# Performance work log

Measured on AMD Instinct MI355X. Metric: run time of the kernel, lower is better.

## Reference

```python
import jax, jax.numpy as jnp
import numpy as np

N, D, E, K = 8192, 1024, 16, 2
CAP = 1024  # capacity_per_expert


def setup_inputs() -> dict:
    key = jax.random.key(0)
    k1, k2, k3 = jax.random.split(key, 3)
    return {
        "moe_inp": jax.random.normal(k1, (N, D), dtype=jnp.float32),
        "gate_w": jax.random.normal(k2, (D, E), dtype=jnp.float32) * 0.02,
        "gate_b": jnp.zeros((E,), dtype=jnp.float32),
        "expert_w": jax.random.normal(k3, (E, D, D), dtype=jnp.float32) * 0.02,
        "expert_b": jnp.zeros((E, D), dtype=jnp.float32),
    }


def _capacity_keep_mask(expert_id, slot_score, num_experts, capacity):
    """For each flattened (token, k) slot assigned to an expert, keep only the
    `capacity` slots with the highest token score (gate_score.max over k),
    matching the argsort-based drop in _fmoe_limited_global_forward."""
    nslots = expert_id.shape[0]
    # sort slots by (expert asc, score desc)
    order = jnp.lexsort((-slot_score, expert_id))
    counts = jnp.bincount(expert_id, length=num_experts)
    starts = jnp.concatenate([jnp.zeros((1,), counts.dtype), jnp.cumsum(counts)[:-1]])
    pos_in_expert = jnp.arange(nslots) - starts[expert_id[order]]
    keep_sorted = pos_in_expert < capacity
    return jnp.zeros((nslots,), dtype=bool).at[order].set(keep_sorted)


def reference(moe_inp, gate_w, gate_b, expert_w, expert_b):
    n, d = moe_inp.shape
    e = expert_w.shape[0]
    # NaiveGate: linear -> top-k -> softmax over the k selected logits
    logits = moe_inp @ gate_w + gate_b                       # [N, E]
    top_v, top_i = jax.lax.top_k(logits, K)                  # [N, K]
    gate_score = jax.nn.softmax(top_v, axis=-1)              # [N, K]

    expert_id = top_i.reshape(-1)                            # [N*K]
    token_id = jnp.arange(n * K) // K                        # [N*K]
    mask_scores = gate_score.max(axis=-1)                    # [N] per-token score
    slot_score = mask_scores[token_id]                       # [N*K]

    keep = _capacity_keep_mask(expert_id, slot_score, e, CAP).reshape(n, K)

    # expert forward: FMoELinear y = x @ W_e^T + b_e (dense over experts, then gather)
    all_out = jnp.einsum('nd,efd->nef', moe_inp, expert_w) + expert_b  # [N, E, D]
    y = jnp.take_along_axis(all_out, top_i[:, :, None], axis=1)        # [N, K, D]
    # dropped (over-capacity) slots pass the scattered input through unchanged
    y = jnp.where(keep[:, :, None], y, moe_inp[:, None, :])
    # combine: bmm(gate_score [N,1,K], y [N,K,D]) -> [N, D]
    return jnp.einsum('nk,nkd->nd', gate_score, y)
```

## Files before the change

kernel.cpp:

```cpp
#include <hip/hip_runtime.h>
#include <hip/hip_bf16.h>
#include <math.h>

#define N_TOK 8192
#define DIM   1024
#define NEXP  16
#define TOPK  2
#define CAPE  1024
#define NSLOT (N_TOK*TOPK)

typedef __attribute__((ext_vector_type(8))) short     short8;
typedef __attribute__((ext_vector_type(4))) float     floatx4;
typedef __attribute__((ext_vector_type(4))) unsigned short ushort4v;

__device__ __forceinline__ unsigned short f2bf(float f) {
    unsigned u = __float_as_uint(f);
    u += 0x7FFFu + ((u >> 16) & 1u);
    return (unsigned short)(u >> 16);
}

#define GLOAD_LDS16(g, l) __builtin_amdgcn_global_load_lds( \
    (const __attribute__((address_space(1))) unsigned int*)(g), \
    (__attribute__((address_space(3))) unsigned int*)(l), 16, 0, 0)

__global__ void gwt_kernel(const float* __restrict__ gw, float* __restrict__ gwT) {
    int i = blockIdx.x * 256 + threadIdx.x;
    if (i >= DIM * NEXP) return;
    int d = i >> 4, e = i & 15;
    gwT[e * DIM + d] = gw[i];
}

__global__ __launch_bounds__(256) void gate_kernel(
        const float* __restrict__ x,
        const float* __restrict__ gwT,
        const float* __restrict__ gb,
        int* __restrict__ slot_expert,
        unsigned long long* __restrict__ slot_key,
        float* __restrict__ slot_gate,
        unsigned short* __restrict__ Xb) {
    const int t    = blockIdx.x * 4 + (threadIdx.x >> 6);
    const int lane = threadIdx.x & 63;

    const floatx4* xr = (const floatx4*)(x + (size_t)t * DIM);
    ushort4v* Xb4 = (ushort4v*)Xb + (size_t)t * 256;
    floatx4 xv[4];
#pragma unroll
    for (int i = 0; i < 4; i++) {
        xv[i] = xr[lane + i * 64];
        ushort4v o;
        o[0] = f2bf(xv[i][0]); o[1] = f2bf(xv[i][1]);
        o[2] = f2bf(xv[i][2]); o[3] = f2bf(xv[i][3]);
        Xb4[lane + i * 64] = o;
    }

    float acc[NEXP];
#pragma unroll
    for (int e = 0; e < NEXP; e++) {
        const floatx4* wr = (const floatx4*)(gwT + (size_t)e * DIM);
        float a = 0.f;
#pragma unroll
        for (int i = 0; i < 4; i++) {
            floatx4 w = wr[lane + i * 64];
            a += xv[i][0]*w[0] + xv[i][1]*w[1] + xv[i][2]*w[2] + xv[i][3]*w[3];
        }
        acc[e] = a;
    }
#pragma unroll
    for (int off = 32; off > 0; off >>= 1) {
#pragma unroll
        for (int e = 0; e < NEXP; e++) acc[e] += __shfl_down(acc[e], off, 64);
    }
    if (lane == 0) {
        float v0 = -1e30f; int i0 = 0;
#pragma unroll
        for (int e = 0; e < NEXP; e++) {
            float v = acc[e] + gb[e];
            acc[e] = v;
            if (v > v0) { v0 = v; i0 = e; }
        }
        float v1 = -1e30f; int i1 = 0;
#pragma unroll
        for (int e = 0; e < NEXP; e++) {
            if (e != i0 && acc[e] > v1) { v1 = acc[e]; i1 = e; }
        }
        float e1 = expf(v1 - v0);
        float den = 1.f + e1;
        float g0 = 1.f / den;
        float g1 = e1 / den;
        unsigned sb = __float_as_uint(g0);
        int s0 = 2 * t, s1 = 2 * t + 1;
        slot_expert[s0] = i0; slot_expert[s1] = i1;
        slot_gate[s0]   = g0; slot_gate[s1]   = g1;
        unsigned long long hi = ((unsigned long long)sb) << 32;
        slot_key[s0] = hi | (unsigned)(0xFFFFFFFFu - (unsigned)s0);
        slot_key[s1] = hi | (unsigned)(0xFFFFFFFFu - (unsigned)s1);
    }
}

__global__ __launch_bounds__(256) void bucket_kernel(
        const int* __restrict__ slot_expert,
        const unsigned long long* __restrict__ slot_key,
        int* __restrict__ counts,
        unsigned long long* __restrict__ buckets) {
    __shared__ int lcnt[NEXP];
    __shared__ int lbase[NEXP];
    const int tid = threadIdx.x;
    const int s = blockIdx.x * 256 + tid;
    if (tid < NEXP) lcnt[tid] = 0;
    __syncthreads();
    const int e = slot_expert[s];
    const unsigned long long key = slot_key[s];
    const int lpos = atomicAdd(&lcnt[e], 1);
    __syncthreads();
    if (tid < NEXP) lbase[tid] = lcnt[tid] ? atomicAdd(&counts[tid], lcnt[tid]) : 0;
    __syncthreads();
    buckets[(size_t)e * NSLOT + lbase[e] + lpos] = key;
}

__global__ __launch_bounds__(256) void keep_wave_kernel(
        const int* __restrict__ slot_expert,
        const unsigned long long* __restrict__ slot_key,
        const int* __restrict__ counts,
        const unsigned long long* __restrict__ buckets,
        int* __restrict__ slot_keep) {
    const int wv   = threadIdx.x >> 6;
    const int lane = threadIdx.x & 63;
    const int s    = blockIdx.x * 4 + wv;
    const int e    = slot_expert[s];
    const int c    = counts[e];
    int kp = 1;
    if (c > CAPE) {
        const unsigned long long k = slot_key[s];
        const unsigned long long* bk = buckets + (size_t)e * NSLOT;
        int rank = 0;
        for (int i = lane; i < c; i += 64) rank += (bk[i] > k) ? 1 : 0;
#pragma unroll
        for (int off = 32; off > 0; off >>= 1) rank += __shfl_down(rank, off, 64);
        kp = (__shfl(rank, 0, 64) < CAPE) ? 1 : 0;
    }
    if (lane == 0) slot_keep[s] = kp;
}

__global__ __launch_bounds__(256) void compact_kernel(
        const int* __restrict__ slot_expert,
        const int* __restrict__ slot_keep,
        int* __restrict__ ecount,
        int* __restrict__ elist,
        int* __restrict__ slot_pos) {
    __shared__ int lcnt[NEXP];
    __shared__ int lbase[NEXP];
    const int tid = threadIdx.x;
    const int s = blockIdx.x * 256 + tid;
    if (tid < NEXP) lcnt[tid] = 0;
    __syncthreads();
    const int e  = slot_expert[s];
    const int kp = slot_keep[s];
    int lpos = 0;
    if (kp) lpos = atomicAdd(&lcnt[e], 1);
    __syncthreads();
    if (tid < NEXP) lbase[tid] = lcnt[tid] ? atomicAdd(&ecount[tid], lcnt[tid]) : 0;
    __syncthreads();
    if (kp) {
        int p = lbase[e] + lpos;
        elist[e * CAPE + p] = s;
        if (slot_pos) slot_pos[s] = e * CAPE + p;
    }
}

__global__ void base_kernel(const float* __restrict__ x,
                            const int* __restrict__ keep,
                            const float* __restrict__ gate,
                            float* __restrict__ out) {
    int i = blockIdx.x * blockDim.x + threadIdx.x;
    int t = i >> 8;
    float c = 0.f;
    if (!keep[2 * t])     c += gate[2 * t];
    if (!keep[2 * t + 1]) c += gate[2 * t + 1];
    floatx4 v = ((const floatx4*)x)[i];
    ((floatx4*)out)[i] = v * c;
}

__global__ void cvt_kernel(const float* __restrict__ src,
                           unsigned short* __restrict__ dst, int n4) {
    int i = blockIdx.x * blockDim.x + threadIdx.x;
    if (i >= n4) return;
    floatx4 v = ((const floatx4*)src)[i];
    ushort4v o;
    o[0] = f2bf(v[0]); o[1] = f2bf(v[1]); o[2] = f2bf(v[2]); o[3] = f2bf(v[3]);
    ((ushort4v*)dst)[i] = o;
}

template <bool STORE_YS>
__global__ __launch_bounds__(256)
void moe_gemm(const unsigned short* __restrict__ Xb,
              const unsigned short* __restrict__ Wb,
              const float* __restrict__ eb,
              const int* __restrict__ elist,
              const int* __restrict__ ecount,
              const float* __restrict__ slot_gate,
              float* __restrict__ ys,
              float* __restrict__ out) {
    __shared__ unsigned short As[128 * 32];
    __shared__ unsigned short Bs[128 * 32];

    const int e  = blockIdx.z;
    const int ne = ecount[e];
    const int m0 = blockIdx.y * 128;
    if (m0 >= ne) return;
    const int n0   = blockIdx.x * 128;
    const int wv   = threadIdx.x >> 6;
    const int lane = threadIdx.x & 63;
    const int q    = lane >> 4;
    const int l15  = lane & 15;

    const int jblk = (lane & 3) ^ ((lane >> 3) & 3);
    const unsigned short* gA[2];
    const unsigned short* gB[2];
    int chunk[2];
#pragma unroll
    for (int c = 0; c < 2; c++) {
        int ch = wv * 2 + c;
        chunk[c] = ch;
        int arow = ch * 16 + (lane >> 2);
        int m    = m0 + arow;
        int slot = elist[e * CAPE + (m < ne ? m : 0)];
        int tok  = slot >> 1;
        gA[c] = Xb + (size_t)tok * DIM + jblk * 8;
        int frow = n0 + arow;
        gB[c] = Wb + (size_t)e * DIM * DIM + (size_t)frow * DIM + jblk * 8;
    }

    const int wm = (wv & 1) * 64;
    const int wn = (wv >> 1) * 64;
    const int kswz = ((l15 >> 1) & 3);
    floatx4 acc[4][4] = {};

    for (int k0 = 0; k0 < DIM; k0 += 32) {
        __syncthreads();
#pragma unroll
        for (int c = 0; c < 2; c++) {
            GLOAD_LDS16(gA[c] + k0, &As[chunk[c] * 512]);
            GLOAD_LDS16(gB[c] + k0, &Bs[chunk[c] * 512]);
        }
        __syncthreads();

        short8 af[4], bf[4];
        const int koff = (q ^ kswz) * 8;
#pragma unroll
        for (int fi = 0; fi < 4; fi++)
            af[fi] = *(const short8*)&As[(wm + fi * 16 + l15) * 32 + koff];
#pragma unroll
        for (int fj = 0; fj < 4; fj++)
            bf[fj] = *(const short8*)&Bs[(wn + fj * 16 + l15) * 32 + koff];
#pragma unroll
        for (int fi = 0; fi < 4; fi++)
#pragma unroll
            for (int fj = 0; fj < 4; fj++)
                acc[fi][fj] = __builtin_amdgcn_mfma_f32_16x16x32_bf16(
                    af[fi], bf[fj], acc[fi][fj], 0, 0, 0);
    }

    float ebv[4];
#pragma unroll
    for (int fj = 0; fj < 4; fj++)
        ebv[fj] = eb[e * DIM + n0 + wn + fj * 16 + l15];
#pragma unroll
    for (int fi = 0; fi < 4; fi++) {
        const int mrow = m0 + wm + fi * 16 + q * 4;
#pragma unroll
        for (int r = 0; r < 4; r++) {
            int m = mrow + r;
            if (m >= ne) continue;
            if (STORE_YS) {
                float* yrow = ys + ((size_t)e * CAPE + m) * DIM + n0 + wn;
#pragma unroll
                for (int fj = 0; fj < 4; fj++)
                    yrow[fj * 16 + l15] = acc[fi][fj][r] + ebv[fj];
            } else {
                int slot = elist[e * CAPE + m];
                int tok  = slot >> 1;
                float g  = slot_gate[slot];
                float* orow = out + (size_t)tok * DIM + n0 + wn;
#pragma unroll
                for (int fj = 0; fj < 4; fj++)
                    atomicAdd(orow + fj * 16 + l15, g * (acc[fi][fj][r] + ebv[fj]));
            }
        }
    }
}

__global__ void combine_kernel(const float* __restrict__ x,
                               const float* __restrict__ ys,
                               const int* __restrict__ keep,
                               const int* __restrict__ pos,
                               const float* __restrict__ gate,
                               float* __restrict__ out) {
    int i = blockIdx.x * 256 + threadIdx.x;
    int t = i >> 8;
    int c = i & 255;
    int s0 = 2 * t, s1 = s0 + 1;
    floatx4 xv = ((const floatx4*)x)[i];
    float g0 = gate[s0], g1 = gate[s1];
    floatx4 r;
    if (keep[s0]) {
        floatx4 y0 = ((const floatx4*)ys)[((size_t)pos[s0] << 8) + c];
        r = y0 * g0;
    } else r = xv * g0;
    if (keep[s1]) {
        floatx4 y1 = ((const floatx4*)ys)[((size_t)pos[s1] << 8) + c];
        r += y1 * g1;
    } else r += xv * g1;
    ((floatx4*)out)[i] = r;
}

extern "C" void kernel_launch(void* const* d_in, const int* in_sizes, int n_in,
                              void* d_out, int out_size, void* d_ws, size_t ws_size,
                              hipStream_t stream) {
    const float* x  = (const float*)d_in[0];
    const float* gw = (const float*)d_in[1];
    const float* gb = (const float*)d_in[2];
    const float* ew = (const float*)d_in[3];
    const float* eb = (const float*)d_in[4];
    float* out = (float*)d_out;

    char* ws = (char*)d_ws;
    int* counts      = (int*)(ws + 0);
    int* ecount      = (int*)(ws + 64);
    int* slot_expert = (int*)(ws + 256);
    int* slot_keep   = (int*)(ws + 65792);
    float* slot_gate = (float*)(ws + 131328);
    unsigned long long* slot_key = (unsigned long long*)(ws + 196864);
    unsigned long long* buckets  = (unsigned long long*)(ws + 327936);
    int* elist       = (int*)(ws + 2425088);
    float* gwT       = (float*)(ws + 2490624);
    unsigned short* Xb = (unsigned short*)(ws + 2556160);
    unsigned short* Wb = (unsigned short*)(ws + 19333376);
    int* slot_pos    = (int*)(ws + 52887808);
    int* ecount2     = (int*)(ws + 52953088);
    float* ys        = (float*)(ws + 52953344);
    const size_t WS_NEED_YS = 52953344ull + (size_t)NEXP * CAPE * DIM * 4;

    const bool ys_path = (ws_size >= WS_NEED_YS);
    (void)ecount2;

    hipMemsetAsync(ws, 0, 256, stream);

    gwt_kernel <<<64, 256, 0, stream>>>(gw, gwT);
    gate_kernel<<<N_TOK / 4, 256, 0, stream>>>(x, gwT, gb, slot_expert, slot_key,
                                               slot_gate, Xb);
    bucket_kernel<<<NSLOT / 256, 256, 0, stream>>>(slot_expert, slot_key, counts, buckets);
    keep_wave_kernel<<<NSLOT / 4, 256, 0, stream>>>(slot_expert, slot_key, counts,
                                                    buckets, slot_keep);
    compact_kernel<<<NSLOT / 256, 256, 0, stream>>>(slot_expert, slot_keep, ecount, elist,
                                                    ys_path ? slot_pos : nullptr);
    cvt_kernel<<<(NEXP * DIM * DIM / 4) / 256, 256, 0, stream>>>(ew, Wb, NEXP * DIM * DIM / 4);

    if (ys_path) {
        moe_gemm<true><<<dim3(8, 8, 16), 256, 0, stream>>>(Xb, Wb, eb, elist, ecount,
                                                           slot_gate, ys, out);
        combine_kernel<<<N_TOK, 256, 0, stream>>>(x, ys, slot_keep, slot_pos,
                                                  slot_gate, out);
    } else {
        base_kernel<<<(N_TOK * DIM / 4) / 256, 256, 0, stream>>>(x, slot_keep,
                                                                 slot_gate, out);
        moe_gemm<false><<<dim3(8, 8, 16), 256, 0, stream>>>(Xb, Wb, eb, elist, ecount,
                                                            slot_gate, nullptr, out);
    }
}
```

Baseline: 266.1 us.

## Rewrite expert GEMM with 256x256 tiles, double-buffered LDS, and interleaved MFMA scheduling

The expert GEMM moves from 128x128 tiles with K=32 and a single LDS buffer to 256x256 tiles with K=64, 512 threads and two LDS buffers. Global-to-LDS loads for the next k-step are issued between MFMA phases, using raw s_barrier, explicit vmcnt waits and s_setprio, so loads overlap compute. The larger tiles cut global reloads of X and W per FLOP but use 128 KB of LDS, more accumulator registers, and give a grid of only 256 blocks, which risks low occupancy and wave underutilisation. A new XOR swizzle is applied on the 64-wide rows to avoid LDS bank conflicts.

```diff
diff --git a/kernel.cpp b/kernel.cpp
--- a/kernel.cpp
+++ b/kernel.cpp
@@ -22,6 +22,8 @@
 #define GLOAD_LDS16(g, l) __builtin_amdgcn_global_load_lds( \
     (const __attribute__((address_space(1))) unsigned int*)(g), \
     (__attribute__((address_space(3))) unsigned int*)(l), 16, 0, 0)
+
+#define RAW_BARRIER() asm volatile("s_barrier" ::: "memory")
 
 __global__ void gwt_kernel(const float* __restrict__ gw, float* __restrict__ gwT) {
     int i = blockIdx.x * 256 + threadIdx.x;
@@ -191,7 +193,7 @@
 }
 
 template <bool STORE_YS>
-__global__ __launch_bounds__(256)
+__global__ __launch_bounds__(512, 2)
 void moe_gemm(const unsigned short* __restrict__ Xb,
               const unsigned short* __restrict__ Wb,
               const float* __restrict__ eb,
@@ -200,79 +202,157 @@
               const float* __restrict__ slot_gate,
               float* __restrict__ ys,
               float* __restrict__ out) {
-    __shared__ unsigned short As[128 * 32];
-    __shared__ unsigned short Bs[128 * 32];
+    __shared__ unsigned short As[2][256 * 64];
+    __shared__ unsigned short Bs[2][256 * 64];
 
     const int e  = blockIdx.z;
     const int ne = ecount[e];
-    const int m0 = blockIdx.y * 128;
+    const int m0 = blockIdx.y * 256;
     if (m0 >= ne) return;
-    const int n0   = blockIdx.x * 128;
-    const int wv   = threadIdx.x >> 6;
-    const int lane = threadIdx.x & 63;
+    const int n0   = blockIdx.x * 256;
+    const int tid  = threadIdx.x;
+    const int wv   = tid >> 6;
+    const int lane = tid & 63;
     const int q    = lane >> 4;
     const int l15  = lane & 15;
-
-    const int jblk = (lane & 3) ^ ((lane >> 3) & 3);
-    const unsigned short* gA[2];
-    const unsigned short* gB[2];
-    int chunk[2];
-#pragma unroll
-    for (int c = 0; c < 2; c++) {
-        int ch = wv * 2 + c;
-        chunk[c] = ch;
-        int arow = ch * 16 + (lane >> 2);
+    const int wr   = wv & 1;
+    const int wc   = wv >> 1;
+
+    const int srow = wv * 8 + (lane >> 3);
+    const int jsrc = (lane & 7) ^ (srow & 7);
+    const unsigned short* gA[4];
+    const unsigned short* gB[4];
+#pragma unroll
+    for (int g = 0; g < 4; g++) {
+        int arow = g * 64 + srow;
         int m    = m0 + arow;
         int slot = elist[e * CAPE + (m < ne ? m : 0)];
-        int tok  = slot >> 1;
-        gA[c] = Xb + (size_t)tok * DIM + jblk * 8;
-        int frow = n0 + arow;
-        gB[c] = Wb + (size_t)e * DIM * DIM + (size_t)frow * DIM + jblk * 8;
-    }
-
-    const int wm = (wv & 1) * 64;
-    const int wn = (wv >> 1) * 64;
-    const int kswz = ((l15 >> 1) & 3);
-    floatx4 acc[4][4] = {};
-
-    for (int k0 = 0; k0 < DIM; k0 += 32) {
-        __syncthreads();
-#pragma unroll
-        for (int c = 0; c < 2; c++) {
-            GLOAD_LDS16(gA[c] + k0, &As[chunk[c] * 512]);
-            GLOAD_LDS16(gB[c] + k0, &Bs[chunk[c] * 512]);
-        }
-        __syncthreads();
-
-        short8 af[4], bf[4];
-        const int koff = (q ^ kswz) * 8;
+        gA[g] = Xb + (size_t)(slot >> 1) * DIM + jsrc * 8;
+        gB[g] = Wb + (size_t)e * DIM * DIM + (size_t)(n0 + arow) * DIM + jsrc * 8;
+    }
+
+#define STAGE_A4(b, k0) do { \
+    GLOAD_LDS16(gA[0] + (k0), &As[b][0 * 4096 + wv * 512]); \
+    GLOAD_LDS16(gA[1] + (k0), &As[b][1 * 4096 + wv * 512]); \
+    GLOAD_LDS16(gA[2] + (k0), &As[b][2 * 4096 + wv * 512]); \
+    GLOAD_LDS16(gA[3] + (k0), &As[b][3 * 4096 + wv * 512]); } while (0)
+#define STAGE_B2(b, g0, k0) do { \
+    GLOAD_LDS16(gB[g0] + (k0),     &Bs[b][(g0) * 4096 + wv * 512]); \
+    GLOAD_LDS16(gB[(g0)+1] + (k0), &Bs[b][((g0)+1) * 4096 + wv * 512]); } while (0)
+
+    STAGE_A4(0, 0);
+    STAGE_B2(0, 0, 0); STAGE_B2(0, 2, 0);
+    STAGE_A4(1, 64);
+    asm volatile("s_waitcnt vmcnt(4)" ::: "memory");
+    __builtin_amdgcn_sched_barrier(0);
+    RAW_BARRIER();
+
+    const int swz0 = (q ^ (l15 & 7)) * 8;
+    const int swz1 = ((4 + q) ^ (l15 & 7)) * 8;
+    const int arow_s = (wr * 128 + l15) * 64;
+    const int brow_s = (wc * 64 + l15) * 64;
+
+    floatx4 acc[8][4] = {};
+    short8 a[4][2], b[4][2];
+
+    for (int t = 0; t < 16; t++) {
+        const unsigned short* A_ = &As[t & 1][0];
+        const unsigned short* B_ = &Bs[t & 1][0];
+        const int nb = (t & 1) ^ 1;
+        const int k1 = (t + 1) * 64;
+        const int k2 = (t + 2) * 64;
+
+#pragma unroll
+        for (int fi = 0; fi < 4; fi++) {
+            a[fi][0] = *(const short8*)(A_ + arow_s + fi * 1024 + swz0);
+            a[fi][1] = *(const short8*)(A_ + arow_s + fi * 1024 + swz1);
+        }
+#pragma unroll
+        for (int fj = 0; fj < 2; fj++) {
+            b[fj][0] = *(const short8*)(B_ + brow_s + fj * 1024 + swz0);
+            b[fj][1] = *(const short8*)(B_ + brow_s + fj * 1024 + swz1);
+        }
+        if (t + 1 < 16) STAGE_B2(nb, 0, k1);
+        RAW_BARRIER();
+        __builtin_amdgcn_s_setprio(1);
 #pragma unroll
         for (int fi = 0; fi < 4; fi++)
-            af[fi] = *(const short8*)&As[(wm + fi * 16 + l15) * 32 + koff];
-#pragma unroll
-        for (int fj = 0; fj < 4; fj++)
-            bf[fj] = *(const short8*)&Bs[(wn + fj * 16 + l15) * 32 + koff];
+#pragma unroll
+            for (int fj = 0; fj < 2; fj++) {
+                acc[fi][fj] = __builtin_amdgcn_mfma_f32_16x16x32_bf16(
+                    a[fi][0], b[fj][0], acc[fi][fj], 0, 0, 0);
+                acc[fi][fj] = __builtin_amdgcn_mfma_f32_16x16x32_bf16(
+                    a[fi][1], b[fj][1], acc[fi][fj], 0, 0, 0);
+            }
+        __builtin_amdgcn_s_setprio(0);
+        RAW_BARRIER();
+
+#pragma unroll
+        for (int fj = 2; fj < 4; fj++) {
+            b[fj][0] = *(const short8*)(B_ + brow_s + fj * 1024 + swz0);
+            b[fj][1] = *(const short8*)(B_ + brow_s + fj * 1024 + swz1);
+        }
+        if (t + 1 < 16) STAGE_B2(nb, 2, k1);
+        RAW_BARRIER();
+        __builtin_amdgcn_s_setprio(1);
 #pragma unroll
         for (int fi = 0; fi < 4; fi++)
 #pragma unroll
-            for (int fj = 0; fj < 4; fj++)
+            for (int fj = 2; fj < 4; fj++) {
                 acc[fi][fj] = __builtin_amdgcn_mfma_f32_16x16x32_bf16(
-                    af[fi], bf[fj], acc[fi][fj], 0, 0, 0);
-    }
+                    a[fi][0], b[fj][0], acc[fi][fj], 0, 0, 0);
+                acc[fi][fj] = __builtin_amdgcn_mfma_f32_16x16x32_bf16(
+                    a[fi][1], b[fj][1], acc[fi][fj], 0, 0, 0);
+            }
+        __builtin_amdgcn_s_setprio(0);
+        RAW_BARRIER();
+
+#pragma unroll
+        for (int fi = 0; fi < 4; fi++) {
+            a[fi][0] = *(const short8*)(A_ + arow_s + 4096 + fi * 1024 + swz0);
+            a[fi][1] = *(const short8*)(A_ + arow_s + 4096 + fi * 1024 + swz1);
+        }
+        RAW_BARRIER();
+        __builtin_amdgcn_s_setprio(1);
+#pragma unroll
+        for (int fi = 0; fi < 4; fi++)
+#pragma unroll
+            for (int fj = 0; fj < 4; fj++) {
+                acc[fi + 4][fj] = __builtin_amdgcn_mfma_f32_16x16x32_bf16(
+                    a[fi][0], b[fj][0], acc[fi + 4][fj], 0, 0, 0);
+                acc[fi + 4][fj] = __builtin_amdgcn_mfma_f32_16x16x32_bf16(
+                    a[fi][1], b[fj][1], acc[fi + 4][fj], 0, 0, 0);
+            }
+        __builtin_amdgcn_s_setprio(0);
+        RAW_BARRIER();
+
+        if (t + 1 < 16) {
+            if (t + 2 < 16) {
+                STAGE_A4(t & 1, k2);
+                asm volatile("s_waitcnt vmcnt(4)" ::: "memory");
+            } else {
+                asm volatile("s_waitcnt vmcnt(0)" ::: "memory");
+            }
+            __builtin_amdgcn_sched_barrier(0);
+            RAW_BARRIER();
+        }
+    }
+#undef STAGE_A4
+#undef STAGE_B2
 
     float ebv[4];
 #pragma unroll
     for (int fj = 0; fj < 4; fj++)
-        ebv[fj] = eb[e * DIM + n0 + wn + fj * 16 + l15];
-#pragma unroll
-    for (int fi = 0; fi < 4; fi++) {
-        const int mrow = m0 + wm + fi * 16 + q * 4;
+        ebv[fj] = eb[e * DIM + n0 + wc * 64 + fj * 16 + l15];
+#pragma unroll
+    for (int fi = 0; fi < 8; fi++) {
+        const int mrow = m0 + wr * 128 + fi * 16 + q * 4;
 #pragma unroll
         for (int r = 0; r < 4; r++) {
             int m = mrow + r;
             if (m >= ne) continue;
             if (STORE_YS) {
-                float* yrow = ys + ((size_t)e * CAPE + m) * DIM + n0 + wn;
+                float* yrow = ys + ((size_t)e * CAPE + m) * DIM + n0 + wc * 64;
 #pragma unroll
                 for (int fj = 0; fj < 4; fj++)
                     yrow[fj * 16 + l15] = acc[fi][fj][r] + ebv[fj];
@@ -280,7 +360,7 @@
                 int slot = elist[e * CAPE + m];
                 int tok  = slot >> 1;
                 float g  = slot_gate[slot];
-                float* orow = out + (size_t)tok * DIM + n0 + wn;
+                float* orow = out + (size_t)tok * DIM + n0 + wc * 64;
 #pragma unroll
                 for (int fj = 0; fj < 4; fj++)
                     atomicAdd(orow + fj * 16 + l15, g * (acc[fi][fj][r] + ebv[fj]));
@@ -356,14 +436,14 @@
     cvt_kernel<<<(NEXP * DIM * DIM / 4) / 256, 256, 0, stream>>>(ew, Wb, NEXP * DIM * DIM / 4);
 
     if (ys_path) {
-        moe_gemm<true><<<dim3(8, 8, 16), 256, 0, stream>>>(Xb, Wb, eb, elist, ecount,
+        moe_gemm<true><<<dim3(4, 4, 16), 512, 0, stream>>>(Xb, Wb, eb, elist, ecount,
                                                            slot_gate, ys, out);
         combine_kernel<<<N_TOK, 256, 0, stream>>>(x, ys, slot_keep, slot_pos,
                                                   slot_gate, out);
     } else {
         base_kernel<<<(N_TOK * DIM / 4) / 256, 256, 0, stream>>>(x, slot_keep,
                                                                  slot_gate, out);
-        moe_gemm<false><<<dim3(8, 8, 16), 256, 0, stream>>>(Xb, Wb, eb, elist, ecount,
+        moe_gemm<false><<<dim3(4, 4, 16), 512, 0, stream>>>(Xb, Wb, eb, elist, ecount,
                                                             slot_gate, nullptr, out);
     }
 }
```

Result: faster. 244.5 us (-8.1%).

## Double-buffer MoE GEMM LDS tiles with 256x128 blocks of 8 waves

Applied to the files above, without the earlier changes.

Rewrites the expert GEMM main loop to double-buffer A/B tiles in LDS, keeping two stages of global-to-LDS loads in flight using explicit vmcnt waits and raw barriers. The block tile grows to 256 rows by 128 columns with 512 threads (8 waves), which halves the grid's M dimension and doubles reuse of each weight tile. MFMA sections are given higher wave priority. LDS use doubles, and the hand-written waitcnt/barrier ordering is fragile if the compiler reorders loads.

```diff
diff --git a/kernel.cpp b/kernel.cpp
--- a/kernel.cpp
+++ b/kernel.cpp
@@ -22,6 +22,8 @@
 #define GLOAD_LDS16(g, l) __builtin_amdgcn_global_load_lds( \
     (const __attribute__((address_space(1))) unsigned int*)(g), \
     (__attribute__((address_space(3))) unsigned int*)(l), 16, 0, 0)
+
+#define RAW_BARRIER() asm volatile("s_barrier" ::: "memory")
 
 __global__ void gwt_kernel(const float* __restrict__ gw, float* __restrict__ gwT) {
     int i = blockIdx.x * 256 + threadIdx.x;
@@ -191,7 +193,7 @@
 }
 
 template <bool STORE_YS>
-__global__ __launch_bounds__(256)
+__global__ __launch_bounds__(512, 4)
 void moe_gemm(const unsigned short* __restrict__ Xb,
               const unsigned short* __restrict__ Wb,
               const float* __restrict__ eb,
@@ -200,65 +202,79 @@
               const float* __restrict__ slot_gate,
               float* __restrict__ ys,
               float* __restrict__ out) {
-    __shared__ unsigned short As[128 * 32];
-    __shared__ unsigned short Bs[128 * 32];
+    __shared__ unsigned short As[2][256 * 32];
+    __shared__ unsigned short Bs[2][128 * 32];
 
     const int e  = blockIdx.z;
     const int ne = ecount[e];
-    const int m0 = blockIdx.y * 128;
+    const int m0 = blockIdx.y * 256;
     if (m0 >= ne) return;
     const int n0   = blockIdx.x * 128;
-    const int wv   = threadIdx.x >> 6;
-    const int lane = threadIdx.x & 63;
+    const int tid  = threadIdx.x;
+    const int wv   = tid >> 6;
+    const int lane = tid & 63;
     const int q    = lane >> 4;
     const int l15  = lane & 15;
-
-    const int jblk = (lane & 3) ^ ((lane >> 3) & 3);
-    const unsigned short* gA[2];
-    const unsigned short* gB[2];
-    int chunk[2];
-#pragma unroll
-    for (int c = 0; c < 2; c++) {
-        int ch = wv * 2 + c;
-        chunk[c] = ch;
-        int arow = ch * 16 + (lane >> 2);
-        int m    = m0 + arow;
+    const int wm   = (wv >> 1) * 64;
+    const int wn   = (wv & 1) * 64;
+
+    const int srow = wv * 16 + (lane >> 2);
+    const int jsrc = (lane & 3) ^ ((lane >> 3) & 3);
+    const unsigned short* gA0;
+    const unsigned short* gA1;
+    {
+        int m = m0 + srow;
         int slot = elist[e * CAPE + (m < ne ? m : 0)];
-        int tok  = slot >> 1;
-        gA[c] = Xb + (size_t)tok * DIM + jblk * 8;
-        int frow = n0 + arow;
-        gB[c] = Wb + (size_t)e * DIM * DIM + (size_t)frow * DIM + jblk * 8;
-    }
-
-    const int wm = (wv & 1) * 64;
-    const int wn = (wv >> 1) * 64;
-    const int kswz = ((l15 >> 1) & 3);
+        gA0 = Xb + (size_t)(slot >> 1) * DIM + jsrc * 8;
+        m = m0 + 128 + srow;
+        slot = elist[e * CAPE + (m < ne ? m : 0)];
+        gA1 = Xb + (size_t)(slot >> 1) * DIM + jsrc * 8;
+    }
+    const unsigned short* gB0 =
+        Wb + (size_t)e * DIM * DIM + (size_t)(n0 + srow) * DIM + jsrc * 8;
+
+#define STAGE(b, k0) do { \
+    GLOAD_LDS16(gA0 + (k0), &As[b][(wv * 16) * 32]); \
+    GLOAD_LDS16(gA1 + (k0), &As[b][(128 + wv * 16) * 32]); \
+    GLOAD_LDS16(gB0 + (k0), &Bs[b][(wv * 16) * 32]); } while (0)
+
+    STAGE(0, 0);
+    STAGE(1, 32);
+
+    const int swz  = (q ^ ((l15 >> 1) & 3)) * 8;
+    const int aoff = (wm + l15) * 32 + swz;
+    const int boff = (wn + l15) * 32 + swz;
+
     floatx4 acc[4][4] = {};
-
-    for (int k0 = 0; k0 < DIM; k0 += 32) {
-        __syncthreads();
-#pragma unroll
-        for (int c = 0; c < 2; c++) {
-            GLOAD_LDS16(gA[c] + k0, &As[chunk[c] * 512]);
-            GLOAD_LDS16(gB[c] + k0, &Bs[chunk[c] * 512]);
-        }
-        __syncthreads();
-
-        short8 af[4], bf[4];
-        const int koff = (q ^ kswz) * 8;
-#pragma unroll
-        for (int fi = 0; fi < 4; fi++)
-            af[fi] = *(const short8*)&As[(wm + fi * 16 + l15) * 32 + koff];
-#pragma unroll
-        for (int fj = 0; fj < 4; fj++)
-            bf[fj] = *(const short8*)&Bs[(wn + fj * 16 + l15) * 32 + koff];
+    short8 a[4], b[4];
+
+    for (int t = 0; t < 32; t++) {
+        const int cur = t & 1;
+        if (t == 31) { asm volatile("s_waitcnt vmcnt(0)" ::: "memory"); }
+        else         { asm volatile("s_waitcnt vmcnt(3)" ::: "memory"); }
+        __builtin_amdgcn_sched_barrier(0);
+        RAW_BARRIER();
+
+        const unsigned short* A_ = &As[cur][0];
+        const unsigned short* B_ = &Bs[cur][0];
+#pragma unroll
+        for (int fi = 0; fi < 4; fi++) a[fi] = *(const short8*)(A_ + aoff + fi * 512);
+#pragma unroll
+        for (int fj = 0; fj < 4; fj++) b[fj] = *(const short8*)(B_ + boff + fj * 512);
+
+        __builtin_amdgcn_s_setprio(1);
 #pragma unroll
         for (int fi = 0; fi < 4; fi++)
 #pragma unroll
             for (int fj = 0; fj < 4; fj++)
                 acc[fi][fj] = __builtin_amdgcn_mfma_f32_16x16x32_bf16(
-                    af[fi], bf[fj], acc[fi][fj], 0, 0, 0);
-    }
+                    a[fi], b[fj], acc[fi][fj], 0, 0, 0);
+        __builtin_amdgcn_s_setprio(0);
+        RAW_BARRIER();
+
+        if (t + 2 < 32) STAGE(cur, (t + 2) * 32);
+    }
+#undef STAGE
 
     float ebv[4];
 #pragma unroll
@@ -356,14 +372,14 @@
     cvt_kernel<<<(NEXP * DIM * DIM / 4) / 256, 256, 0, stream>>>(ew, Wb, NEXP * DIM * DIM / 4);
 
     if (ys_path) {
-        moe_gemm<true><<<dim3(8, 8, 16), 256, 0, stream>>>(Xb, Wb, eb, elist, ecount,
+        moe_gemm<true><<<dim3(8, 4, 16), 512, 0, stream>>>(Xb, Wb, eb, elist, ecount,
                                                            slot_gate, ys, out);
         combine_kernel<<<N_TOK, 256, 0, stream>>>(x, ys, slot_keep, slot_pos,
                                                   slot_gate, out);
     } else {
         base_kernel<<<(N_TOK * DIM / 4) / 256, 256, 0, stream>>>(x, slot_keep,
                                                                  slot_gate, out);
-        moe_gemm<false><<<dim3(8, 8, 16), 256, 0, stream>>>(Xb, Wb, eb, elist, ecount,
+        moe_gemm<false><<<dim3(8, 4, 16), 512, 0, stream>>>(Xb, Wb, eb, elist, ecount,
                                                             slot_gate, nullptr, out);
     }
 }
```

New measurement: 243.8 us. -8.4%, faster.
